# Optimization experiments

Measured on AMD Instinct MI355X. Metric: run time of the kernel, lower is better.

## Reference

```python
import jax, jax.numpy as jnp
import numpy as np

N, D = 8192, 2        # n_samples, embedding dim (== init dim)
K = 32                # k_base with strategy='fixed' -> static topk size
ALPHA = 1.0           # alpha.item() in forward -> constant
NOISE_SCALE = 0.01
EPS = 1e-8


def setup_inputs() -> dict:
    key = jax.random.key(0)
    x = jax.random.normal(key, (N, D), dtype=jnp.float32)
    return {"x": x}


def _forward(x):
    # torch.std is unbiased (ddof=1)
    mean = jnp.mean(x, axis=0, keepdims=True)          # [1, D]
    std = jnp.std(x, axis=0, keepdims=True, ddof=1)    # [1, D]
    xc = x - mean

    # pairwise Euclidean distances (torch.cdist, p=2): [N, N]
    sq = jnp.sum(xc * xc, axis=1)
    d2 = sq[:, None] + sq[None, :] - 2.0 * (xc @ xc.T)
    dists = jnp.sqrt(jnp.maximum(d2, 0.0))

    # kth-smallest distance per row -> per-point bandwidth sigma
    neg_topk, _ = jax.lax.top_k(-dists, K)             # smallest K (incl. self)
    sigma = -neg_topk[:, -1][:, None]                  # [N, 1]

    # adaptive-bandwidth kernel, row-normalized
    kernel = jnp.exp(-dists / (2.0 * sigma ** 2 + EPS))
    kernel = kernel / (jnp.sum(kernel, axis=1, keepdims=True) + EPS)

    drift = kernel @ xc                                # [N, D]

    step = float(D) ** (-ALPHA)                        # dim ** (-alpha)
    noise = jax.random.normal(jax.random.key(42), xc.shape, dtype=xc.dtype) * NOISE_SCALE
    h = xc + step * (drift - xc) + noise

    # restore original per-feature scale and location
    cur_std = jnp.std(h, axis=0, keepdims=True, ddof=1)
    h = h * (std / (cur_std + EPS))
    return h + mean


def reference(x):
    return _forward(x)
```

## Files before the change

### kernel.cpp

```cpp
#include <hip/hip_runtime.h>
#include <stdint.h>
#include <math.h>

#define N_PTS 8192
#define WPB   8
#define TPB   (WPB * 64)
#define NBLK  (N_PTS / WPB)
#define AITER (N_PTS / 64 / 4)

typedef __fp16 h2 __attribute__((ext_vector_type(2)));
typedef uint32_t u32;

__device__ __forceinline__ u32 pkmin(u32 a, u32 b) {
  u32 d; asm("v_pk_min_f16 %0, %1, %2" : "=v"(d) : "v"(a), "v"(b)); return d;
}
__device__ __forceinline__ u32 pkmax(u32 a, u32 b) {
  u32 d; asm("v_pk_max_f16 %0, %1, %2" : "=v"(d) : "v"(a), "v"(b)); return d;
}
__device__ __forceinline__ u32 pksub(u32 a, u32 b) {
  u32 d;
  asm("v_pk_add_f16 %0, %1, %2 neg_lo:[0,1] neg_hi:[0,1]" : "=v"(d) : "v"(a), "v"(b));
  return d;
}
__device__ __forceinline__ float dot2u(u32 a, u32 b, float c) {
  return __builtin_amdgcn_fdot2(__builtin_bit_cast(h2, a), __builtin_bit_cast(h2, b), c, false);
}
__device__ __forceinline__ u32 cvtpk(float a, float b) {
  return __builtin_bit_cast(u32, __builtin_amdgcn_cvt_pkrtz(a, b));
}

__device__ __forceinline__ uint32_t rotl32(uint32_t x, int r) {
  return (x << r) | (x >> (32 - r));
}

__device__ __forceinline__ uint32_t threefry_bits(uint32_t idx) {
  const uint32_t k0 = 0u, k1 = 42u;
  const uint32_t k2c = k0 ^ k1 ^ 0x1BD11BDAu;
  uint32_t x0 = 0u, x1 = idx;
  x0 += k0; x1 += k1;
  x0 += x1; x1 = rotl32(x1, 13); x1 ^= x0;
  x0 += x1; x1 = rotl32(x1, 15); x1 ^= x0;
  x0 += x1; x1 = rotl32(x1, 26); x1 ^= x0;
  x0 += x1; x1 = rotl32(x1,  6); x1 ^= x0;
  x0 += k1; x1 += k2c + 1u;
  x0 += x1; x1 = rotl32(x1, 17); x1 ^= x0;
  x0 += x1; x1 = rotl32(x1, 29); x1 ^= x0;
  x0 += x1; x1 = rotl32(x1, 16); x1 ^= x0;
  x0 += x1; x1 = rotl32(x1, 24); x1 ^= x0;
  x0 += k2c; x1 += k0 + 2u;
  x0 += x1; x1 = rotl32(x1, 13); x1 ^= x0;
  x0 += x1; x1 = rotl32(x1, 15); x1 ^= x0;
  x0 += x1; x1 = rotl32(x1, 26); x1 ^= x0;
  x0 += x1; x1 = rotl32(x1,  6); x1 ^= x0;
  x0 += k0; x1 += k1 + 3u;
  x0 += x1; x1 = rotl32(x1, 17); x1 ^= x0;
  x0 += x1; x1 = rotl32(x1, 29); x1 ^= x0;
  x0 += x1; x1 = rotl32(x1, 16); x1 ^= x0;
  x0 += x1; x1 = rotl32(x1, 24); x1 ^= x0;
  x0 += k1; x1 += k2c + 4u;
  x0 += x1; x1 = rotl32(x1, 13); x1 ^= x0;
  x0 += x1; x1 = rotl32(x1, 15); x1 ^= x0;
  x0 += x1; x1 = rotl32(x1, 26); x1 ^= x0;
  x0 += x1; x1 = rotl32(x1,  6); x1 ^= x0;
  x0 += k2c; x1 += k0 + 5u;
  return x0 ^ x1;
}

__device__ __forceinline__ float erfinv_xla(float x) {
  float w = -log1pf(-x * x);
  float p;
  if (w < 5.0f) {
    w -= 2.5f;
    p = 2.81022636e-08f;
    p = fmaf(p, w, 3.43273939e-07f);
    p = fmaf(p, w, -3.5233877e-06f);
    p = fmaf(p, w, -4.39150654e-06f);
    p = fmaf(p, w, 0.00021858087f);
    p = fmaf(p, w, -0.00125372503f);
    p = fmaf(p, w, -0.00417768164f);
    p = fmaf(p, w, 0.246640727f);
    p = fmaf(p, w, 1.50140941f);
  } else {
    w = sqrtf(w) - 3.0f;
    p = -0.000200214257f;
    p = fmaf(p, w, 0.000100950558f);
    p = fmaf(p, w, 0.00134934322f);
    p = fmaf(p, w, -0.00367342844f);
    p = fmaf(p, w, 0.00573950773f);
    p = fmaf(p, w, -0.0076224613f);
    p = fmaf(p, w, 0.00943887047f);
    p = fmaf(p, w, 1.00167406f);
    p = fmaf(p, w, 2.83297682f);
  }
  return p * x;
}

__device__ __forceinline__ float jax_noise(uint32_t idx) {
  uint32_t bits = threefry_bits(idx);
  float uf = __uint_as_float((bits >> 9) | 0x3F800000u) - 1.0f;
  const float lo_u = -0.99999994f;
  float u = fmaxf(lo_u, fmaf(uf, 2.0f, lo_u));
  return 1.4142135623730951f * erfinv_xla(u) * 0.01f;
}

__global__ __launch_bounds__(TPB, 8) void main_kernel(const float* __restrict__ x,
                                                      float* __restrict__ stats,
                                                      float* __restrict__ h_out,
                                                      double* __restrict__ partials) {
  __shared__ u32 xs[N_PTS];
  __shared__ double sred[WPB][4];
  __shared__ float sbc[2];

  const int t = threadIdx.x;
  const int w = t >> 6;
  const int s = t & 63;
  const int row = blockIdx.x * WPB + w;

  const float2 xg = ((const float2*)x)[row];
  const u32 xihu = cvtpk(xg.x, xg.y);

  const float4* x4 = (const float4*)x;
  double s0 = 0, s1 = 0, q0 = 0, q1 = 0;
#pragma unroll
  for (int k = 0; k < N_PTS / 2 / TPB; ++k) {
    float4 v = x4[k * TPB + t];
    ((uint2*)xs)[k * TPB + t] = make_uint2(cvtpk(v.x, v.y), cvtpk(v.z, v.w));
    s0 += (double)v.x + (double)v.z;
    s1 += (double)v.y + (double)v.w;
    q0 += fma((double)v.x, (double)v.x, (double)v.z * (double)v.z);
    q1 += fma((double)v.y, (double)v.y, (double)v.w * (double)v.w);
  }
#pragma unroll
  for (int m = 1; m < 64; m <<= 1) {
    s0 += __shfl_xor(s0, m); s1 += __shfl_xor(s1, m);
    q0 += __shfl_xor(q0, m); q1 += __shfl_xor(q1, m);
  }
  if (s == 0) { sred[w][0] = s0; sred[w][1] = s1; sred[w][2] = q0; sred[w][3] = q1; }
  __syncthreads();
  if (t == 0) {
    double a0 = 0, a1 = 0, b0 = 0, b1 = 0;
#pragma unroll
    for (int k = 0; k < WPB; ++k) {
      a0 += sred[k][0]; a1 += sred[k][1]; b0 += sred[k][2]; b1 += sred[k][3];
    }
    double n = (double)N_PTS;
    double m0 = a0 / n, m1 = a1 / n;
    sbc[0] = (float)m0; sbc[1] = (float)m1;
    if (blockIdx.x == 0) {
      stats[0] = (float)m0;
      stats[1] = (float)m1;
      stats[2] = (float)sqrt((b0 - n * m0 * m0) / (n - 1.0));
      stats[3] = (float)sqrt((b1 - n * m1 * m1) / (n - 1.0));
    }
  }

  u32 r0[4], r1[4];
#pragma unroll
  for (int k = 0; k < 4; ++k) { r0[k] = 0x7C007C00u; r1[k] = 0x7C007C00u; }

  const uint4* xsv = (const uint4*)xs;
  __syncthreads();
#pragma unroll 8
  for (int tt = 0; tt < AITER; ++tt) {
    uint4 q = xsv[tt * 64 + s];
    u32 e0 = pksub(xihu, q.x);
    u32 e1 = pksub(xihu, q.y);
    u32 e2 = pksub(xihu, q.z);
    u32 e3 = pksub(xihu, q.w);
    u32 e01 = cvtpk(dot2u(e0, e0, 0.0f), dot2u(e1, e1, 0.0f));
    u32 e23 = cvtpk(dot2u(e2, e2, 0.0f), dot2u(e3, e3, 0.0f));
    r0[3] = pkmin(pkmax(r0[2], e01), r0[3]);
    r0[2] = pkmin(pkmax(r0[1], e01), r0[2]);
    r0[1] = pkmin(pkmax(r0[0], e01), r0[1]);
    r0[0] = pkmin(r0[0], e01);
    r1[3] = pkmin(pkmax(r1[2], e23), r1[3]);
    r1[2] = pkmin(pkmax(r1[1], e23), r1[2]);
    r1[1] = pkmin(pkmax(r1[0], e23), r1[1]);
    r1[0] = pkmin(r1[0], e23);
  }

  u32 lo[8], hi[8];
#pragma unroll
  for (int k = 0; k < 4; ++k) {
    lo[k] = r0[k] & 0xFFFFu; hi[k] = r0[k] >> 16;
    lo[4 + k] = r1[k] & 0xFFFFu; hi[4 + k] = r1[k] >> 16;
  }
  u32 blo = 0u, bhi = 0x7C01u;
  for (int it = 0; it < 15; ++it) {
    u32 mid = (blo + bhi) >> 1;
    int c = 0;
#pragma unroll
    for (int k = 0; k < 8; ++k) {
      c += __popcll(__ballot(lo[k] < mid));
      c += __popcll(__ballot(hi[k] < mid));
    }
    bool ge = (c >= 32);
    bhi = ge ? mid : bhi;
    blo = ge ? blo : mid;
  }
  unsigned short v32 = (unsigned short)(bhi - 1u);
  float d2k = (float)__builtin_bit_cast(__fp16, v32);
  float den = fmaf(2.0f, d2k, 1e-8f);
  float nc1 = -1.4426950408889634f / den;

  const u32 one2 = 0x3C003C00u;
  float sw = 0.f, swx = 0.f, swy = 0.f;
#pragma unroll 4
  for (int tt = 0; tt < AITER; ++tt) {
    uint4 q = xsv[tt * 64 + s];
    u32 e0 = pksub(xihu, q.x);
    u32 e1 = pksub(xihu, q.y);
    u32 e2 = pksub(xihu, q.z);
    u32 e3 = pksub(xihu, q.w);
    float d0 = __builtin_amdgcn_sqrtf(dot2u(e0, e0, 0.0f));
    float d1 = __builtin_amdgcn_sqrtf(dot2u(e1, e1, 0.0f));
    float d2 = __builtin_amdgcn_sqrtf(dot2u(e2, e2, 0.0f));
    float d3 = __builtin_amdgcn_sqrtf(dot2u(e3, e3, 0.0f));
    float w0 = __builtin_amdgcn_exp2f(fmaf(nc1, d0, 10.0f));
    float w1 = __builtin_amdgcn_exp2f(fmaf(nc1, d1, 10.0f));
    float w2 = __builtin_amdgcn_exp2f(fmaf(nc1, d2, 10.0f));
    float w3 = __builtin_amdgcn_exp2f(fmaf(nc1, d3, 10.0f));
    u32 wh01 = cvtpk(w0, w1);
    u32 wh23 = cvtpk(w2, w3);
    u32 xx01 = __builtin_amdgcn_perm(q.y, q.x, 0x05040100u);
    u32 yy01 = __builtin_amdgcn_perm(q.y, q.x, 0x07060302u);
    u32 xx23 = __builtin_amdgcn_perm(q.w, q.z, 0x05040100u);
    u32 yy23 = __builtin_amdgcn_perm(q.w, q.z, 0x07060302u);
    sw  = dot2u(wh01, one2, sw);  sw  = dot2u(wh23, one2, sw);
    swx = dot2u(wh01, xx01, swx); swx = dot2u(wh23, xx23, swx);
    swy = dot2u(wh01, yy01, swy); swy = dot2u(wh23, yy23, swy);
  }
#pragma unroll
  for (int m = 1; m < 64; m <<= 1) {
    sw  += __shfl_xor(sw,  m);
    swx += __shfl_xor(swx, m);
    swy += __shfl_xor(swy, m);
  }

  __syncthreads();
  float* hrow = (float*)xs;
  if (s < 2) {
    const float mean = sbc[s];
    float inv   = 1.0f / (sw + 1e-8f);
    float drift = (s == 0 ? swx : swy) * inv - mean;
    float xcv   = (s == 0 ? xg.x : xg.y) - mean;
    uint32_t idx = 2u * (uint32_t)row + (uint32_t)s;
    float h = fmaf(0.5f, drift - xcv, xcv) + jax_noise(idx);
    h_out[idx] = h;
    hrow[w * 2 + s] = h;
  }
  __syncthreads();
  if (t < 2) {
    double sm = 0.0, sq = 0.0;
#pragma unroll
    for (int k = 0; k < WPB; ++k) {
      double v = (double)hrow[k * 2 + t];
      sm += v; sq += v * v;
    }
    partials[blockIdx.x * 4 + t]     = sm;
    partials[blockIdx.x * 4 + 2 + t] = sq;
  }
}

__global__ __launch_bounds__(256) void scalefinal_kernel(const double* __restrict__ partials,
                                                         const float* __restrict__ stats,
                                                         float* __restrict__ h) {
  __shared__ double red[256][4];
  __shared__ float sc[2];
  const int t = threadIdx.x;
  double a0 = 0, a1 = 0, a2 = 0, a3 = 0;
#pragma unroll
  for (int kb = 0; kb < NBLK / 256; ++kb) {
    int b = kb * 256 + t;
    a0 += partials[b * 4 + 0]; a1 += partials[b * 4 + 1];
    a2 += partials[b * 4 + 2]; a3 += partials[b * 4 + 3];
  }
  red[t][0] = a0; red[t][1] = a1; red[t][2] = a2; red[t][3] = a3;
  __syncthreads();
  for (int st = 128; st > 0; st >>= 1) {
    if (t < st) {
      red[t][0] += red[t + st][0]; red[t][1] += red[t + st][1];
      red[t][2] += red[t + st][2]; red[t][3] += red[t + st][3];
    }
    __syncthreads();
  }
  if (t < 2) {
    double n = (double)N_PTS;
    double m = red[0][t] / n;
    double v = (red[0][2 + t] - n * m * m) / (n - 1.0);
    sc[t] = stats[2 + t] / ((float)sqrt(v) + 1e-8f);
  }
  __syncthreads();
  int i = blockIdx.x * 256 + t;
  int d = i & 1;
  h[i] = fmaf(h[i], sc[d], stats[d]);
}

extern "C" void kernel_launch(void* const* d_in, const int* in_sizes, int n_in,
                              void* d_out, int out_size, void* d_ws, size_t ws_size,
                              hipStream_t stream) {
  const float* x = (const float*)d_in[0];
  float* out = (float*)d_out;
  float* stats = (float*)d_ws;
  double* partials = (double*)((char*)d_ws + 64);

  main_kernel<<<NBLK, TPB, 0, stream>>>(x, stats, out, partials);
  scalefinal_kernel<<<16384 / 256, 256, 0, stream>>>(partials, stats, out);
}
```

Measured before the change: 54.09 us.

## Use uniform spatial grid for kNN bandwidth and truncated kernel sums

Points are binned into a 64x64 grid via count, prefix-sum, placement and stable rank kernels, producing cell-sorted fp16 points. Each row finds its 32nd-nearest distance by scanning an expanding cell window until the result is certified by the window margin. It then accumulates kernel weights only over cells within a cutoff radius, replacing the all-pairs scans. This adds several small serial launches and atomics, and drops negligible far-field weights, which is an approximation.

New measurement: 94.11 us. +74.0%, slower.

```diff
diff --git a/kernel.cpp b/kernel.cpp
--- a/kernel.cpp
+++ b/kernel.cpp
@@ -6,33 +6,38 @@
 #define WPB   8
 #define TPB   (WPB * 64)
 #define NBLK  (N_PTS / WPB)
-#define AITER (N_PTS / 64 / 4)
+#define GRIDC 64
+#define NCELL (GRIDC * GRIDC)
+#define CW    (9.0f / 64.0f)
+#define CINV  (64.0f / 9.0f)
 
 typedef __fp16 h2 __attribute__((ext_vector_type(2)));
 typedef uint32_t u32;
 
-__device__ __forceinline__ u32 pkmin(u32 a, u32 b) {
-  u32 d; asm("v_pk_min_f16 %0, %1, %2" : "=v"(d) : "v"(a), "v"(b)); return d;
-}
-__device__ __forceinline__ u32 pkmax(u32 a, u32 b) {
-  u32 d; asm("v_pk_max_f16 %0, %1, %2" : "=v"(d) : "v"(a), "v"(b)); return d;
-}
 __device__ __forceinline__ u32 pksub(u32 a, u32 b) {
   u32 d;
   asm("v_pk_add_f16 %0, %1, %2 neg_lo:[0,1] neg_hi:[0,1]" : "=v"(d) : "v"(a), "v"(b));
   return d;
 }
 __device__ __forceinline__ float dot2u(u32 a, u32 b, float c) {
+#if __has_builtin(__builtin_amdgcn_fdot2)
   return __builtin_amdgcn_fdot2(__builtin_bit_cast(h2, a), __builtin_bit_cast(h2, b), c, false);
+#else
+  h2 x = __builtin_bit_cast(h2, a), y = __builtin_bit_cast(h2, b);
+  return fmaf((float)x.x, (float)y.x, fmaf((float)x.y, (float)y.y, c));
+#endif
 }
 __device__ __forceinline__ u32 cvtpk(float a, float b) {
   return __builtin_bit_cast(u32, __builtin_amdgcn_cvt_pkrtz(a, b));
 }
+__device__ __forceinline__ int cellc(float v) {
+  int c = (int)floorf((v + 4.5f) * CINV);
+  return c < 0 ? 0 : (c > GRIDC - 1 ? GRIDC - 1 : c);
+}
 
 __device__ __forceinline__ uint32_t rotl32(uint32_t x, int r) {
   return (x << r) | (x >> (32 - r));
 }
-
 __device__ __forceinline__ uint32_t threefry_bits(uint32_t idx) {
   const uint32_t k0 = 0u, k1 = 42u;
   const uint32_t k2c = k0 ^ k1 ^ 0x1BD11BDAu;
@@ -65,7 +70,6 @@
   x0 += k2c; x1 += k0 + 5u;
   return x0 ^ x1;
 }
-
 __device__ __forceinline__ float erfinv_xla(float x) {
   float w = -log1pf(-x * x);
   float p;
@@ -94,7 +98,6 @@
   }
   return p * x;
 }
-
 __device__ __forceinline__ float jax_noise(uint32_t idx) {
   uint32_t bits = threefry_bits(idx);
   float uf = __uint_as_float((bits >> 9) | 0x3F800000u) - 1.0f;
@@ -103,132 +106,192 @@
   return 1.4142135623730951f * erfinv_xla(u) * 0.01f;
 }
 
+__global__ __launch_bounds__(256) void count_kernel(const float* __restrict__ x,
+                                                    u32* __restrict__ counts) {
+  int i = blockIdx.x * 256 + threadIdx.x;
+  float2 p = ((const float2*)x)[i];
+  int cell = cellc(p.y) * GRIDC + cellc(p.x);
+  atomicAdd(&counts[cell], 1u);
+}
+
+__global__ __launch_bounds__(1024) void prefix_stats_kernel(const float* __restrict__ x,
+                                                            u32* __restrict__ counts,
+                                                            u32* __restrict__ base,
+                                                            float* __restrict__ stats) {
+  __shared__ u32 ssc[1024];
+  __shared__ double sd[1024][4];
+  const int t = threadIdx.x;
+  u32 c[4]; u32 sum = 0;
+#pragma unroll
+  for (int k = 0; k < 4; ++k) { c[k] = counts[t * 4 + k]; sum += c[k]; }
+  ssc[t] = sum;
+  __syncthreads();
+  for (int off = 1; off < 1024; off <<= 1) {
+    u32 v = (t >= off) ? ssc[t - off] : 0u;
+    __syncthreads();
+    ssc[t] += v;
+    __syncthreads();
+  }
+  u32 run = ssc[t] - sum;
+#pragma unroll
+  for (int k = 0; k < 4; ++k) { base[t * 4 + k] = run; run += c[k]; }
+  if (t == 1023) base[NCELL] = run;
+  __syncthreads();
+#pragma unroll
+  for (int k = 0; k < 4; ++k) counts[t * 4 + k] = base[t * 4 + k];
+
+  double s0 = 0, s1 = 0, q0 = 0, q1 = 0;
+#pragma unroll
+  for (int k = 0; k < 8; ++k) {
+    float2 p = ((const float2*)x)[t * 8 + k];
+    s0 += (double)p.x; s1 += (double)p.y;
+    q0 += (double)p.x * (double)p.x; q1 += (double)p.y * (double)p.y;
+  }
+  sd[t][0] = s0; sd[t][1] = s1; sd[t][2] = q0; sd[t][3] = q1;
+  __syncthreads();
+  for (int off = 512; off > 0; off >>= 1) {
+    if (t < off) {
+      sd[t][0] += sd[t + off][0]; sd[t][1] += sd[t + off][1];
+      sd[t][2] += sd[t + off][2]; sd[t][3] += sd[t + off][3];
+    }
+    __syncthreads();
+  }
+  if (t == 0) {
+    double n = (double)N_PTS;
+    double m0 = sd[0][0] / n, m1 = sd[0][1] / n;
+    stats[0] = (float)m0;
+    stats[1] = (float)m1;
+    stats[2] = (float)sqrt((sd[0][2] - n * m0 * m0) / (n - 1.0));
+    stats[3] = (float)sqrt((sd[0][3] - n * m1 * m1) / (n - 1.0));
+  }
+}
+
+__global__ __launch_bounds__(256) void place_kernel(const float* __restrict__ x,
+                                                    u32* __restrict__ cursor,
+                                                    u32* __restrict__ tmp_pt,
+                                                    u32* __restrict__ tmp_ci) {
+  int i = blockIdx.x * 256 + threadIdx.x;
+  float2 p = ((const float2*)x)[i];
+  int cell = cellc(p.y) * GRIDC + cellc(p.x);
+  u32 slot = atomicAdd(&cursor[cell], 1u);
+  tmp_pt[slot] = cvtpk(p.x, p.y);
+  tmp_ci[slot] = ((u32)cell << 13) | (u32)i;
+}
+
+__global__ __launch_bounds__(256) void rank_kernel(const u32* __restrict__ base,
+                                                   const u32* __restrict__ tmp_pt,
+                                                   const u32* __restrict__ tmp_ci,
+                                                   u32* __restrict__ spt,
+                                                   unsigned short* __restrict__ sidx) {
+  int s = blockIdx.x * 256 + threadIdx.x;
+  u32 v = tmp_ci[s];
+  u32 cell = v >> 13, i = v & 8191u;
+  u32 lo = base[cell], hi = base[cell + 1];
+  u32 rank = 0;
+  for (u32 j = lo; j < hi; ++j) rank += ((tmp_ci[j] & 8191u) < i) ? 1u : 0u;
+  u32 d = lo + rank;
+  spt[d] = tmp_pt[s];
+  sidx[d] = (unsigned short)i;
+}
+
 __global__ __launch_bounds__(TPB, 8) void main_kernel(const float* __restrict__ x,
-                                                      float* __restrict__ stats,
+                                                      const float* __restrict__ stats,
+                                                      const u32* __restrict__ base,
+                                                      const u32* __restrict__ spt,
+                                                      const unsigned short* __restrict__ sidx,
                                                       float* __restrict__ h_out,
                                                       double* __restrict__ partials) {
-  __shared__ u32 xs[N_PTS];
-  __shared__ double sred[WPB][4];
-  __shared__ float sbc[2];
-
+  __shared__ float hrow[WPB * 2];
   const int t = threadIdx.x;
   const int w = t >> 6;
   const int s = t & 63;
-  const int row = blockIdx.x * WPB + w;
-
-  const float2 xg = ((const float2*)x)[row];
+  const int p = blockIdx.x * WPB + w;
+  const int orig = (int)sidx[p];
+  const float2 xg = ((const float2*)x)[orig];
   const u32 xihu = cvtpk(xg.x, xg.y);
-
-  const float4* x4 = (const float4*)x;
-  double s0 = 0, s1 = 0, q0 = 0, q1 = 0;
-#pragma unroll
-  for (int k = 0; k < N_PTS / 2 / TPB; ++k) {
-    float4 v = x4[k * TPB + t];
-    ((uint2*)xs)[k * TPB + t] = make_uint2(cvtpk(v.x, v.y), cvtpk(v.z, v.w));
-    s0 += (double)v.x + (double)v.z;
-    s1 += (double)v.y + (double)v.w;
-    q0 += fma((double)v.x, (double)v.x, (double)v.z * (double)v.z);
-    q1 += fma((double)v.y, (double)v.y, (double)v.w * (double)v.w);
-  }
-#pragma unroll
-  for (int m = 1; m < 64; m <<= 1) {
-    s0 += __shfl_xor(s0, m); s1 += __shfl_xor(s1, m);
-    q0 += __shfl_xor(q0, m); q1 += __shfl_xor(q1, m);
-  }
-  if (s == 0) { sred[w][0] = s0; sred[w][1] = s1; sred[w][2] = q0; sred[w][3] = q1; }
-  __syncthreads();
-  if (t == 0) {
-    double a0 = 0, a1 = 0, b0 = 0, b1 = 0;
-#pragma unroll
-    for (int k = 0; k < WPB; ++k) {
-      a0 += sred[k][0]; a1 += sred[k][1]; b0 += sred[k][2]; b1 += sred[k][3];
-    }
-    double n = (double)N_PTS;
-    double m0 = a0 / n, m1 = a1 / n;
-    sbc[0] = (float)m0; sbc[1] = (float)m1;
-    if (blockIdx.x == 0) {
-      stats[0] = (float)m0;
-      stats[1] = (float)m1;
-      stats[2] = (float)sqrt((b0 - n * m0 * m0) / (n - 1.0));
-      stats[3] = (float)sqrt((b1 - n * m1 * m1) / (n - 1.0));
-    }
-  }
-
-  u32 r0[4], r1[4];
-#pragma unroll
-  for (int k = 0; k < 4; ++k) { r0[k] = 0x7C007C00u; r1[k] = 0x7C007C00u; }
-
-  const uint4* xsv = (const uint4*)xs;
-  __syncthreads();
-#pragma unroll 8
-  for (int tt = 0; tt < AITER; ++tt) {
-    uint4 q = xsv[tt * 64 + s];
-    u32 e0 = pksub(xihu, q.x);
-    u32 e1 = pksub(xihu, q.y);
-    u32 e2 = pksub(xihu, q.z);
-    u32 e3 = pksub(xihu, q.w);
-    u32 e01 = cvtpk(dot2u(e0, e0, 0.0f), dot2u(e1, e1, 0.0f));
-    u32 e23 = cvtpk(dot2u(e2, e2, 0.0f), dot2u(e3, e3, 0.0f));
-    r0[3] = pkmin(pkmax(r0[2], e01), r0[3]);
-    r0[2] = pkmin(pkmax(r0[1], e01), r0[2]);
-    r0[1] = pkmin(pkmax(r0[0], e01), r0[1]);
-    r0[0] = pkmin(r0[0], e01);
-    r1[3] = pkmin(pkmax(r1[2], e23), r1[3]);
-    r1[2] = pkmin(pkmax(r1[1], e23), r1[2]);
-    r1[1] = pkmin(pkmax(r1[0], e23), r1[1]);
-    r1[0] = pkmin(r1[0], e23);
-  }
-
-  u32 lo[8], hi[8];
-#pragma unroll
-  for (int k = 0; k < 4; ++k) {
-    lo[k] = r0[k] & 0xFFFFu; hi[k] = r0[k] >> 16;
-    lo[4 + k] = r1[k] & 0xFFFFu; hi[4 + k] = r1[k] >> 16;
-  }
-  u32 blo = 0u, bhi = 0x7C01u;
-  for (int it = 0; it < 15; ++it) {
-    u32 mid = (blo + bhi) >> 1;
-    int c = 0;
-#pragma unroll
-    for (int k = 0; k < 8; ++k) {
-      c += __popcll(__ballot(lo[k] < mid));
-      c += __popcll(__ballot(hi[k] < mid));
-    }
-    bool ge = (c >= 32);
-    bhi = ge ? mid : bhi;
-    blo = ge ? blo : mid;
-  }
-  unsigned short v32 = (unsigned short)(bhi - 1u);
-  float d2k = (float)__builtin_bit_cast(__fp16, v32);
-  float den = fmaf(2.0f, d2k, 1e-8f);
-  float nc1 = -1.4426950408889634f / den;
-
-  const u32 one2 = 0x3C003C00u;
+  const int cx = cellc(xg.x), cy = cellc(xg.y);
+  const float INF = 3.402823466e+38f;
+
+  float d2k;
+  int r = 2;
+  for (;;) {
+    float r0 = INF, r1 = INF, r2 = INF, r3 = INF, r4 = INF, r5 = INF;
+    const int cxl = max(cx - r, 0), cxh = min(cx + r, GRIDC - 1);
+    const int cyl = max(cy - r, 0), cyh = min(cy + r, GRIDC - 1);
+    u32 acc = 0;
+    for (int yy = cyl; yy <= cyh; ++yy) {
+      const int rowb = yy << 6;
+      u32 lo = base[rowb + cxl];
+      u32 len = base[rowb + cxh + 1] - lo;
+      u32 k0 = ((u32)s - acc) & 63u;
+      for (u32 k = k0; k < len; k += 64u) {
+        u32 qp = spt[lo + k];
+        u32 e = pksub(xihu, qp);
+        float d2 = dot2u(e, e, 0.0f);
+        r5 = fminf(fmaxf(r4, d2), r5);
+        r4 = fminf(fmaxf(r3, d2), r4);
+        r3 = fminf(fmaxf(r2, d2), r3);
+        r2 = fminf(fmaxf(r1, d2), r2);
+        r1 = fminf(fmaxf(r0, d2), r1);
+        r0 = fminf(r0, d2);
+      }
+      acc += len;
+    }
+    u32 b0 = (u32)__builtin_bit_cast(unsigned short, (__fp16)r0);
+    u32 b1 = (u32)__builtin_bit_cast(unsigned short, (__fp16)r1);
+    u32 b2 = (u32)__builtin_bit_cast(unsigned short, (__fp16)r2);
+    u32 b3 = (u32)__builtin_bit_cast(unsigned short, (__fp16)r3);
+    u32 b4 = (u32)__builtin_bit_cast(unsigned short, (__fp16)r4);
+    u32 b5 = (u32)__builtin_bit_cast(unsigned short, (__fp16)r5);
+    u32 blo = 0u, bhi = 0x7C01u;
+    for (int it = 0; it < 15; ++it) {
+      u32 mid = (blo + bhi) >> 1;
+      int c = __popcll(__ballot(b0 < mid)) + __popcll(__ballot(b1 < mid)) +
+              __popcll(__ballot(b2 < mid)) + __popcll(__ballot(b3 < mid)) +
+              __popcll(__ballot(b4 < mid)) + __popcll(__ballot(b5 < mid));
+      bool ge = (c >= 32);
+      bhi = ge ? mid : bhi;
+      blo = ge ? blo : mid;
+    }
+    unsigned short v32 = (unsigned short)(bhi - 1u);
+    d2k = (float)__builtin_bit_cast(__fp16, v32);
+
+    float d32 = sqrtf(d2k) + 1e-2f;
+    float mxl = (cxl > 0) ? xg.x - (-4.5f + cxl * CW) : 1e9f;
+    float mxh = (cxh < GRIDC - 1) ? (-4.5f + (cxh + 1) * CW) - xg.x : 1e9f;
+    float myl = (cyl > 0) ? xg.y - (-4.5f + cyl * CW) : 1e9f;
+    float myh = (cyh < GRIDC - 1) ? (-4.5f + (cyh + 1) * CW) - xg.y : 1e9f;
+    float margin = fminf(fminf(mxl, mxh), fminf(myl, myh));
+    if (d32 <= margin) break;
+    r <<= 1;
+  }
+
+  const float den = fmaf(2.0f, d2k, 1e-8f);
+  const float nc1 = -1.4426950408889634f / den;
+  const float dcut = 15.943f * den;
+
   float sw = 0.f, swx = 0.f, swy = 0.f;
-#pragma unroll 4
-  for (int tt = 0; tt < AITER; ++tt) {
-    uint4 q = xsv[tt * 64 + s];
-    u32 e0 = pksub(xihu, q.x);
-    u32 e1 = pksub(xihu, q.y);
-    u32 e2 = pksub(xihu, q.z);
-    u32 e3 = pksub(xihu, q.w);
-    float d0 = __builtin_amdgcn_sqrtf(dot2u(e0, e0, 0.0f));
-    float d1 = __builtin_amdgcn_sqrtf(dot2u(e1, e1, 0.0f));
-    float d2 = __builtin_amdgcn_sqrtf(dot2u(e2, e2, 0.0f));
-    float d3 = __builtin_amdgcn_sqrtf(dot2u(e3, e3, 0.0f));
-    float w0 = __builtin_amdgcn_exp2f(fmaf(nc1, d0, 10.0f));
-    float w1 = __builtin_amdgcn_exp2f(fmaf(nc1, d1, 10.0f));
-    float w2 = __builtin_amdgcn_exp2f(fmaf(nc1, d2, 10.0f));
-    float w3 = __builtin_amdgcn_exp2f(fmaf(nc1, d3, 10.0f));
-    u32 wh01 = cvtpk(w0, w1);
-    u32 wh23 = cvtpk(w2, w3);
-    u32 xx01 = __builtin_amdgcn_perm(q.y, q.x, 0x05040100u);
-    u32 yy01 = __builtin_amdgcn_perm(q.y, q.x, 0x07060302u);
-    u32 xx23 = __builtin_amdgcn_perm(q.w, q.z, 0x05040100u);
-    u32 yy23 = __builtin_amdgcn_perm(q.w, q.z, 0x07060302u);
-    sw  = dot2u(wh01, one2, sw);  sw  = dot2u(wh23, one2, sw);
-    swx = dot2u(wh01, xx01, swx); swx = dot2u(wh23, xx23, swx);
-    swy = dot2u(wh01, yy01, swy); swy = dot2u(wh23, yy23, swy);
+  {
+    const int bxl = cellc(xg.x - dcut), bxh = cellc(xg.x + dcut);
+    const int byl = cellc(xg.y - dcut), byh = cellc(xg.y + dcut);
+    u32 acc = 0;
+    for (int yy = byl; yy <= byh; ++yy) {
+      const int rowb = yy << 6;
+      u32 lo = base[rowb + bxl];
+      u32 len = base[rowb + bxh + 1] - lo;
+      u32 k0 = ((u32)s - acc) & 63u;
+      for (u32 k = k0; k < len; k += 64u) {
+        u32 qp = spt[lo + k];
+        u32 e = pksub(xihu, qp);
+        float d = __builtin_amdgcn_sqrtf(dot2u(e, e, 0.0f));
+        float wgt = __builtin_amdgcn_exp2f(fmaf(nc1, d, 10.0f));
+        h2 ph = __builtin_bit_cast(h2, qp);
+        sw += wgt;
+        swx = fmaf(wgt, (float)ph.x, swx);
+        swy = fmaf(wgt, (float)ph.y, swy);
+      }
+      acc += len;
+    }
   }
 #pragma unroll
   for (int m = 1; m < 64; m <<= 1) {
@@ -237,14 +300,12 @@
     swy += __shfl_xor(swy, m);
   }
 
-  __syncthreads();
-  float* hrow = (float*)xs;
   if (s < 2) {
-    const float mean = sbc[s];
+    const float mean = stats[s];
     float inv   = 1.0f / (sw + 1e-8f);
     float drift = (s == 0 ? swx : swy) * inv - mean;
     float xcv   = (s == 0 ? xg.x : xg.y) - mean;
-    uint32_t idx = 2u * (uint32_t)row + (uint32_t)s;
+    uint32_t idx = 2u * (uint32_t)orig + (uint32_t)s;
     float h = fmaf(0.5f, drift - xcv, xcv) + jax_noise(idx);
     h_out[idx] = h;
     hrow[w * 2 + s] = h;
@@ -301,9 +362,21 @@
                               hipStream_t stream) {
   const float* x = (const float*)d_in[0];
   float* out = (float*)d_out;
-  float* stats = (float*)d_ws;
-  double* partials = (double*)((char*)d_ws + 64);
-
-  main_kernel<<<NBLK, TPB, 0, stream>>>(x, stats, out, partials);
+  char* W = (char*)d_ws;
+  float* stats = (float*)W;
+  u32* counts = (u32*)(W + 128);
+  u32* base   = (u32*)(W + 16512);
+  unsigned short* sidx = (unsigned short*)(W + 33024);
+  u32* tmp_pt = (u32*)(W + 49408);
+  u32* tmp_ci = (u32*)(W + 82176);
+  u32* spt    = (u32*)(W + 114944);
+  double* partials = (double*)(W + 49408);
+
+  hipMemsetAsync(counts, 0, NCELL * sizeof(u32), stream);
+  count_kernel<<<N_PTS / 256, 256, 0, stream>>>(x, counts);
+  prefix_stats_kernel<<<1, 1024, 0, stream>>>(x, counts, base, stats);
+  place_kernel<<<N_PTS / 256, 256, 0, stream>>>(x, counts, tmp_pt, tmp_ci);
+  rank_kernel<<<N_PTS / 256, 256, 0, stream>>>(base, tmp_pt, tmp_ci, spt, sidx);
+  main_kernel<<<NBLK, TPB, 0, stream>>>(x, stats, base, spt, sidx, out, partials);
   scalefinal_kernel<<<16384 / 256, 256, 0, stream>>>(partials, stats, out);
 }
```
